# Kernel optimization log

Hardware: AMD Instinct MI355X
Metric: run time of the kernel (lower is better)

The kernel has to match this reference:

```python
import jax, jax.numpy as jnp
import numpy as np

N = 16384      # nodes per NodeFlow layer
E = 262144     # edges per block (avg degree 16)
T = 327680     # total interpro indices (~20 per node)
P = 20000      # protein embedding table rows
INTERPRO = 30000
D_ESM = 1280
D = 1024
L = 5000       # labels_num
G = 2          # num_gcn


def setup_inputs() -> dict:
    key = jax.random.key(0)
    ks = jax.random.split(key, 16)
    protein_embedding = jax.random.normal(ks[0], (P, D_ESM), jnp.float32) * 0.02
    interpro_weight = jax.random.normal(ks[1], (INTERPRO, D), jnp.float32) * 0.02
    W_esm = jax.random.normal(ks[2], (D, D_ESM), jnp.float32) * (1.0 / np.sqrt(D_ESM))
    b_esm = jnp.zeros((D,), jnp.float32)
    bias1 = jnp.zeros((D,), jnp.float32)
    bias2 = jnp.zeros((D,), jnp.float32)
    w = jnp.ones((2,), jnp.float32)
    W_upd = jax.random.normal(ks[3], (G, D, 2 * D), jnp.float32) * (1.0 / np.sqrt(2 * D))
    b_upd = jnp.zeros((G, D), jnp.float32)
    W_out = jax.random.normal(ks[4], (L, D + D_ESM), jnp.float32) * (1.0 / np.sqrt(D + D_ESM))
    b_out = jnp.zeros((L,), jnp.float32)
    self_w = jax.random.uniform(ks[5], (E,), jnp.float32)
    ppi_w = jax.random.uniform(ks[6], (E,), jnp.float32)
    inputs = jax.random.randint(ks[7], (N,), 0, P)
    interpro_idx = jax.random.randint(ks[8], (T,), 0, INTERPRO)
    off = jnp.sort(jax.random.randint(ks[9], (N + 1,), 0, T))
    interpro_off = off.at[0].set(0).at[-1].set(T)  # include_last_offset convention
    src = jax.random.randint(ks[10], (E,), 0, N)
    dst = jax.random.randint(ks[11], (E,), 0, N)
    target_id = jax.random.randint(ks[12], (N,), 0, P)
    return dict(protein_embedding=protein_embedding, interpro_weight=interpro_weight,
                W_esm=W_esm, b_esm=b_esm, bias1=bias1, bias2=bias2, w=w,
                W_upd=W_upd, b_upd=b_upd, W_out=W_out, b_out=b_out,
                self_w=self_w, ppi_w=ppi_w, inputs=inputs,
                interpro_idx=interpro_idx, interpro_off=interpro_off,
                src=src, dst=dst, target_id=target_id)


def reference(protein_embedding, interpro_weight, W_esm, b_esm, bias1, bias2, w,
              W_upd, b_upd, W_out, b_out, self_w, ppi_w,
              inputs, interpro_idx, interpro_off, src, dst, target_id):
    # x1: ESM branch -> relu(Linear(esm[inputs]) + bias1)
    x1 = jax.nn.relu(protein_embedding[inputs] @ W_esm.T + b_esm + bias1)  # [N, D]
    # x2: EmbeddingBag(mode='sum', include_last_offset=True) + bias2
    seg = jnp.searchsorted(interpro_off, jnp.arange(T), side='right') - 1  # bag id per index
    bags = jax.ops.segment_sum(interpro_weight[interpro_idx], seg, num_segments=N)
    x2 = jax.nn.relu(bags + bias2)  # [N, D]
    # learned softmax mixture of the two branches
    sm = jax.nn.softmax(w)
    h = sm[0] * x1 + sm[1] * x2  # [N, D]
    # message passing layers: u_mul_e + sum for 'self' and 'ppi' edge weights,
    # then NodeUpdate: relu(Linear(cat(ppi_out, res))). Dropout is identity (eval).
    for i in range(G):
        msg = h[src]  # [E, D] irregular gather
        res = jax.ops.segment_sum(msg * self_w[:, None], dst, num_segments=N)
        ppi_out = jax.ops.segment_sum(msg * ppi_w[:, None], dst, num_segments=N)
        h = jax.nn.relu(jnp.concatenate([ppi_out, res], axis=1) @ W_upd[i].T + b_upd[i])
    last = jnp.concatenate([h, protein_embedding[target_id]], axis=1)  # [N, D+D_ESM]
    return last @ W_out.T + b_out  # [N, L]
```

## Files before the change

### kernel.cpp

```cpp
#include <hip/hip_runtime.h>

typedef unsigned short u16;
typedef u16 u16x4 __attribute__((ext_vector_type(4)));
typedef u16 u16x8 __attribute__((ext_vector_type(8)));
typedef float f32x4 __attribute__((ext_vector_type(4)));
typedef __bf16 bf16x8 __attribute__((ext_vector_type(8)));

#define NN 16384
#define EE 262144
#define DD 1024
#define DESM 1280
#define LL 5000
#define IPN 30000

static __device__ __forceinline__ u16 f2bf(float f) {
  unsigned u = __float_as_uint(f);
  u += 0x7FFF + ((u >> 16) & 1);
  return (u16)(u >> 16);
}
static __device__ __forceinline__ float bf2f(u16 h) {
  return __uint_as_float(((unsigned)h) << 16);
}

__global__ void cast_rows_k(const float* __restrict__ src, int scols,
                            const int* __restrict__ rowidx,
                            u16* __restrict__ dst, int dld, int dcol0,
                            int rows, int cols8 ) {
  long total = (long)rows * cols8;
  for (long i = blockIdx.x * (long)blockDim.x + threadIdx.x; i < total;
       i += (long)gridDim.x * blockDim.x) {
    int r = (int)(i / cols8);
    int k8 = (int)(i % cols8);
    int sr = rowidx ? rowidx[r] : r;
    const f32x4* s = (const f32x4*)(src + (size_t)sr * scols + (size_t)k8 * 8);
    f32x4 a = s[0], b = s[1];
    u16x8 o;
    o[0] = f2bf(a[0]); o[1] = f2bf(a[1]); o[2] = f2bf(a[2]); o[3] = f2bf(a[3]);
    o[4] = f2bf(b[0]); o[5] = f2bf(b[1]); o[6] = f2bf(b[2]); o[7] = f2bf(b[3]);
    *(u16x8*)(dst + (size_t)r * dld + dcol0 + (size_t)k8 * 8) = o;
  }
}

__global__ void embed_bag_k(const u16* __restrict__ W, const int* __restrict__ idx,
                            const int* __restrict__ off, const float* __restrict__ bias2,
                            u16* __restrict__ x2b) {
  int node = blockIdx.x * 2 + (threadIdx.x >> 7);
  int t = threadIdx.x & 127;
  int beg = off[node], end = off[node + 1];
  float a[8];
#pragma unroll
  for (int j = 0; j < 8; ++j) a[j] = 0.f;
  int p = beg;
  for (; p + 8 <= end; p += 8) {
    u16x8 v[8];
#pragma unroll
    for (int q = 0; q < 8; ++q)
      v[q] = *(const u16x8*)(W + (size_t)idx[p + q] * DD + t * 8);
#pragma unroll
    for (int q = 0; q < 8; ++q)
#pragma unroll
      for (int j = 0; j < 8; ++j) a[j] += bf2f(v[q][j]);
  }
  for (; p + 2 <= end; p += 2) {
    u16x8 v0 = *(const u16x8*)(W + (size_t)idx[p] * DD + t * 8);
    u16x8 v1 = *(const u16x8*)(W + (size_t)idx[p + 1] * DD + t * 8);
#pragma unroll
    for (int j = 0; j < 8; ++j) a[j] += bf2f(v0[j]) + bf2f(v1[j]);
  }
  if (p < end) {
    u16x8 v0 = *(const u16x8*)(W + (size_t)idx[p] * DD + t * 8);
#pragma unroll
    for (int j = 0; j < 8; ++j) a[j] += bf2f(v0[j]);
  }
  f32x4 b0 = *(const f32x4*)(bias2 + t * 8);
  f32x4 b1 = *(const f32x4*)(bias2 + t * 8 + 4);
  u16x8 o;
#pragma unroll
  for (int j = 0; j < 4; ++j) o[j] = f2bf(fmaxf(a[j] + b0[j], 0.f));
#pragma unroll
  for (int j = 0; j < 4; ++j) o[j + 4] = f2bf(fmaxf(a[j + 4] + b1[j], 0.f));
  *(u16x8*)(x2b + (size_t)node * DD + t * 8) = o;
}

__global__ void hist_k(const int* __restrict__ dst, int* __restrict__ counts) {
  int e = blockIdx.x * blockDim.x + threadIdx.x;
  if (e < EE) atomicAdd(&counts[dst[e]], 1);
}

__global__ void scan_k(const int* __restrict__ counts, int* __restrict__ row_off) {
  __shared__ int sh[256];
  int t = threadIdx.x;
  int s = 0;
  for (int i = 0; i < 64; ++i) s += counts[t * 64 + i];
  sh[t] = s;
  __syncthreads();
  if (t == 0) {
    int run = 0;
    for (int i = 0; i < 256; ++i) { int v = sh[i]; sh[i] = run; run += v; }
    row_off[NN] = run;
  }
  __syncthreads();
  int run = sh[t];
  for (int i = 0; i < 64; ++i) { row_off[t * 64 + i] = run; run += counts[t * 64 + i]; }
}

__global__ void scatter_k(const int* __restrict__ dst, const int* __restrict__ src,
                          const float* __restrict__ selfw, const float* __restrict__ ppiw,
                          int* __restrict__ cursor, int4* __restrict__ rec) {
  int e = blockIdx.x * blockDim.x + threadIdx.x;
  if (e < EE) {
    int pos = atomicAdd(&cursor[dst[e]], 1);
    int4 r;
    r.x = src[e];
    r.y = __float_as_int(selfw[e]);
    r.z = __float_as_int(ppiw[e]);
    r.w = 0;
    rec[pos] = r;
  }
}

__global__ void aggregate_k(const u16* __restrict__ h, const int* __restrict__ row_off,
                            const int4* __restrict__ rec, u16* __restrict__ cat) {
  int node = blockIdx.x * 2 + (threadIdx.x >> 7);
  int t = threadIdx.x & 127;
  int beg = row_off[node], end = row_off[node + 1];
  float res[8], ppi[8];
#pragma unroll
  for (int j = 0; j < 8; ++j) { res[j] = 0.f; ppi[j] = 0.f; }
  int p = beg;
  for (; p + 8 <= end; p += 8) {
    int4 r[8];
    u16x8 m[8];
#pragma unroll
    for (int q = 0; q < 8; ++q) r[q] = rec[p + q];
#pragma unroll
    for (int q = 0; q < 8; ++q)
      m[q] = *(const u16x8*)(h + (size_t)r[q].x * DD + t * 8);
#pragma unroll
    for (int q = 0; q < 8; ++q) {
      float ws = __int_as_float(r[q].y), wp = __int_as_float(r[q].z);
#pragma unroll
      for (int j = 0; j < 8; ++j) {
        float f = bf2f(m[q][j]);
        res[j] += ws * f;
        ppi[j] += wp * f;
      }
    }
  }
  for (; p + 2 <= end; p += 2) {
    int4 r0 = rec[p], r1 = rec[p + 1];
    u16x8 m0 = *(const u16x8*)(h + (size_t)r0.x * DD + t * 8);
    u16x8 m1 = *(const u16x8*)(h + (size_t)r1.x * DD + t * 8);
    float ws0 = __int_as_float(r0.y), wp0 = __int_as_float(r0.z);
    float ws1 = __int_as_float(r1.y), wp1 = __int_as_float(r1.z);
#pragma unroll
    for (int j = 0; j < 8; ++j) {
      float f0 = bf2f(m0[j]), f1 = bf2f(m1[j]);
      res[j] += ws0 * f0 + ws1 * f1;
      ppi[j] += wp0 * f0 + wp1 * f1;
    }
  }
  if (p < end) {
    int4 r0 = rec[p];
    u16x8 m0 = *(const u16x8*)(h + (size_t)r0.x * DD + t * 8);
    float ws = __int_as_float(r0.y), wp = __int_as_float(r0.z);
#pragma unroll
    for (int j = 0; j < 8; ++j) {
      float f = bf2f(m0[j]);
      res[j] += ws * f;
      ppi[j] += wp * f;
    }
  }
  u16x8 o0, o1;
#pragma unroll
  for (int j = 0; j < 8; ++j) { o0[j] = f2bf(ppi[j]); o1[j] = f2bf(res[j]); }
  *(u16x8*)(cat + (size_t)node * 2048 + t * 8) = o0;
  *(u16x8*)(cat + (size_t)node * 2048 + DD + t * 8) = o1;
}

static __device__ __forceinline__ void stage_half(const char* Gb, size_t ldb, int rowbase,
                                                  int rowmax, int kbyte, char* lds_half_w,
                                                  int s_rowoff, int s_inner) {
#pragma unroll
  for (int j = 0; j < 2; ++j) {
    int row = rowbase + j * 128 + s_rowoff;
    if (row > rowmax) row = rowmax;
    const char* src = Gb + (size_t)row * ldb + kbyte + s_inner;
    __builtin_amdgcn_global_load_lds(
        (const __attribute__((address_space(1))) void*)src,
        (__attribute__((address_space(3))) void*)(lds_half_w + j * 8192), 16, 0, 0);
  }
}

static __device__ __forceinline__ bf16x8 ldr(const char* kh, int row, int slot) {
  unsigned a = (unsigned)row * 64u +
               ((((unsigned)slot << 4) ^ ((((unsigned)row >> 1) & 3u) << 4)));
  return *(const bf16x8*)(kh + a);
}

template <int MODE>
__global__ __launch_bounds__(512, 2) void gemm8_k(
    const u16* __restrict__ A, const u16* __restrict__ B, int M, int N, int K,
    void* __restrict__ Cout, int ldc, const float* __restrict__ bias0,
    const float* __restrict__ bias1, const u16* __restrict__ x2b,
    const float* __restrict__ wmix) {
  __shared__ char lds[131072];
  char* ldsA = lds;
  char* ldsB = lds + 65536;
  const int tid = threadIdx.x;
  const int lane = tid & 63;
  const int wid = tid >> 6;
  const int wr = wid >> 2;
  const int wc = wid & 3;
  const int nwg = gridDim.x * gridDim.y;
  const int flat = blockIdx.x + gridDim.x * blockIdx.y;
  const int swz = (flat & 7) * (nwg >> 3) + (flat >> 3);
  const int row0 = (swz / gridDim.x) * 256;
  const int col0 = (swz % gridDim.x) * 256;
  const int NT = K >> 6;
  const size_t lda = (size_t)K * 2;
  const char* Ab = (const char*)A;
  const char* Bb = (const char*)B;
  const int l15 = lane & 15;
  const int slot = lane >> 4;
  const int s_rowoff = wid * 16 + (lane >> 2);
  const int s_inner = (((lane & 3) << 4) ^ (((lane >> 3) & 3) << 4));
  const int wb = wid * 1024;

  f32x4 acc[8][4];
#pragma unroll
  for (int m = 0; m < 8; ++m)
#pragma unroll
    for (int n = 0; n < 4; ++n) acc[m][n] = (f32x4){0.f, 0.f, 0.f, 0.f};

  const int k1 = (NT > 1) ? 128 : 0;
  stage_half(Bb, lda, col0, N - 1, 0,       ldsB + 0     + wb, s_rowoff, s_inner);
  stage_half(Ab, lda, row0, M - 1, 0,       ldsA + 0     + wb, s_rowoff, s_inner);
  stage_half(Ab, lda, row0, M - 1, 64,      ldsA + 16384 + wb, s_rowoff, s_inner);
  stage_half(Bb, lda, col0, N - 1, 64,      ldsB + 16384 + wb, s_rowoff, s_inner);
  stage_half(Bb, lda, col0, N - 1, k1,      ldsB + 32768 + wb, s_rowoff, s_inner);
  stage_half(Ab, lda, row0, M - 1, k1,      ldsA + 32768 + wb, s_rowoff, s_inner);
  stage_half(Bb, lda, col0, N - 1, k1 + 64, ldsB + 49152 + wb, s_rowoff, s_inner);
  asm volatile("s_waitcnt vmcnt(6)" ::: "memory");
  __builtin_amdgcn_s_barrier();

  bf16x8 afP[4], afQ[4], bqP[4], bqQ[4];
#pragma unroll
  for (int m = 0; m < 4; ++m) afP[m] = ldr(ldsA, wr * 128 + m * 16 + l15, slot);
#pragma unroll
  for (int n = 0; n < 4; ++n) bqP[n] = ldr(ldsB, wc * 64 + n * 16 + l15, slot);

  for (int t = 0; t < NT; ++t) {
    const int d = t & 1;
    char* Ad = ldsA + d * 32768;
    char* Bd = ldsB + d * 32768;
    const char* Akh1 = Ad + 16384;
    const char* Bkh1 = Bd + 16384;
    const char* AkhN0 = ldsA + (d ^ 1) * 32768;
    const char* BkhN0 = ldsB + (d ^ 1) * 32768;
    const int ts1 = (t + 1 < NT) ? t + 1 : NT - 1;
    const int ts2 = (t + 2 < NT) ? t + 2 : NT - 1;

#pragma unroll
    for (int m = 0; m < 4; ++m) afQ[m] = ldr(Ad, wr * 128 + (m + 4) * 16 + l15, slot);
#pragma unroll
    for (int n = 0; n < 4; ++n) bqQ[n] = ldr(Bkh1, wc * 64 + n * 16 + l15, slot);
    stage_half(Ab, lda, row0, M - 1, ts1 * 128 + 64,
               ldsA + ((t + 1) & 1) * 32768 + 16384 + wb, s_rowoff, s_inner);
    __builtin_amdgcn_sched_barrier(0);
    __builtin_amdgcn_s_setprio(1);
#pragma unroll
    for (int m = 0; m < 4; ++m)
#pragma unroll
      for (int n = 0; n < 4; ++n)
        acc[m][n] = __builtin_amdgcn_mfma_f32_16x16x32_bf16(afP[m], bqP[n], acc[m][n], 0, 0, 0);
    __builtin_amdgcn_s_setprio(0);
    asm volatile("s_waitcnt vmcnt(8)" ::: "memory");
    __builtin_amdgcn_s_barrier();

#pragma unroll
    for (int m = 0; m < 4; ++m) afP[m] = ldr(Akh1, wr * 128 + (m + 4) * 16 + l15, slot);
    stage_half(Bb, lda, col0, N - 1, ts2 * 128, Bd + wb, s_rowoff, s_inner);
    __builtin_amdgcn_sched_barrier(0);
    __builtin_amdgcn_s_setprio(1);
#pragma unroll
    for (int m = 0; m < 4; ++m)
#pragma unroll
      for (int n = 0; n < 4; ++n)
        acc[m + 4][n] = __builtin_amdgcn_mfma_f32_16x16x32_bf16(afQ[m], bqP[n], acc[m + 4][n], 0, 0, 0);
    __builtin_amdgcn_s_setprio(0);
    __builtin_amdgcn_s_barrier();

#pragma unroll
    for (int m = 0; m < 4; ++m) afQ[m] = ldr(Akh1, wr * 128 + m * 16 + l15, slot);
    stage_half(Ab, lda, row0, M - 1, ts2 * 128, Ad + wb, s_rowoff, s_inner);
    __builtin_amdgcn_sched_barrier(0);
    __builtin_amdgcn_s_setprio(1);
#pragma unroll
    for (int m = 0; m < 4; ++m)
#pragma unroll
      for (int n = 0; n < 4; ++n)
        acc[m + 4][n] = __builtin_amdgcn_mfma_f32_16x16x32_bf16(afP[m], bqQ[n], acc[m + 4][n], 0, 0, 0);
    __builtin_amdgcn_s_setprio(0);
    asm volatile("s_waitcnt vmcnt(6)" ::: "memory");
    __builtin_amdgcn_s_barrier();

#pragma unroll
    for (int m = 0; m < 4; ++m) afP[m] = ldr(AkhN0, wr * 128 + m * 16 + l15, slot);
#pragma unroll
    for (int n = 0; n < 4; ++n) bqP[n] = ldr(BkhN0, wc * 64 + n * 16 + l15, slot);
    stage_half(Bb, lda, col0, N - 1, ts2 * 128 + 64, Bd + 16384 + wb, s_rowoff, s_inner);
    __builtin_amdgcn_sched_barrier(0);
    __builtin_amdgcn_s_setprio(1);
#pragma unroll
    for (int m = 0; m < 4; ++m)
#pragma unroll
      for (int n = 0; n < 4; ++n)
        acc[m][n] = __builtin_amdgcn_mfma_f32_16x16x32_bf16(afQ[m], bqQ[n], acc[m][n], 0, 0, 0);
    __builtin_amdgcn_s_setprio(0);
    __builtin_amdgcn_s_barrier();
  }

  float sm0 = 0.f, sm1 = 0.f;
  if (MODE == 0) {
    float w0 = wmix[0], w1 = wmix[1];
    float mx = fmaxf(w0, w1);
    float e0 = expf(w0 - mx), e1 = expf(w1 - mx);
    float inv = 1.f / (e0 + e1);
    sm0 = e0 * inv;
    sm1 = e1 * inv;
  }
  float bc[4];
  int cs[4];
#pragma unroll
  for (int n = 0; n < 4; ++n) {
    int c = col0 + wc * 64 + n * 16 + l15;
    cs[n] = c;
    bc[n] = (MODE == 2 && c >= N) ? 0.f : (bias0[c] + (MODE == 0 ? bias1[c] : 0.f));
  }
#pragma unroll
  for (int m = 0; m < 8; ++m) {
#pragma unroll
    for (int n = 0; n < 4; ++n) {
      int c = cs[n];
      if (MODE == 2 && c >= N) continue;
      int r0 = row0 + wr * 128 + m * 16 + slot * 4;
#pragma unroll
      for (int r = 0; r < 4; ++r) {
        float v = acc[m][n][r] + bc[n];
        int rr = r0 + r;
        if (MODE == 0) {
          float x1v = fmaxf(v, 0.f);
          float x2v = bf2f(x2b[(size_t)rr * DD + c]);
          ((u16*)Cout)[(size_t)rr * ldc + c] = f2bf(sm0 * x1v + sm1 * x2v);
        } else if (MODE == 1) {
          ((u16*)Cout)[(size_t)rr * ldc + c] = f2bf(fmaxf(v, 0.f));
        } else {
          __builtin_nontemporal_store(v, &((float*)Cout)[(size_t)rr * ldc + c]);
        }
      }
    }
  }
}

extern "C" void kernel_launch(void* const* d_in, const int* in_sizes, int n_in,
                              void* d_out, int out_size, void* d_ws, size_t ws_size,
                              hipStream_t stream) {
  const float* esm   = (const float*)d_in[0];
  const float* ipw   = (const float*)d_in[1];
  const float* Wesm  = (const float*)d_in[2];
  const float* besm  = (const float*)d_in[3];
  const float* bias1 = (const float*)d_in[4];
  const float* bias2 = (const float*)d_in[5];
  const float* wmix  = (const float*)d_in[6];
  const float* Wupd  = (const float*)d_in[7];
  const float* bupd  = (const float*)d_in[8];
  const float* Wout  = (const float*)d_in[9];
  const float* bout  = (const float*)d_in[10];
  const float* selfw = (const float*)d_in[11];
  const float* ppiw  = (const float*)d_in[12];
  const int* inputs  = (const int*)d_in[13];
  const int* ipidx   = (const int*)d_in[14];
  const int* ipoff   = (const int*)d_in[15];
  const int* src     = (const int*)d_in[16];
  const int* dst     = (const int*)d_in[17];
  const int* tgt     = (const int*)d_in[18];
  float* out = (float*)d_out;

  char* ws = (char*)d_ws;
  size_t o = 0;
  auto take = [&](size_t b) {
    char* r = ws + o;
    o += (b + 255) & ~(size_t)255;
    return r;
  };
  u16* Wesm_b = (u16*)take(1024ull * 1280 * 2);
  u16* Wupd_b = (u16*)take(2ull * 1024 * 2048 * 2);
  u16* Wout_b = (u16*)take(5000ull * 2304 * 2);
  int* counts  = (int*)take((size_t)NN * 4);
  int* row_off = (int*)take((size_t)(NN + 1) * 4);
  int* cursor  = (int*)take((size_t)NN * 4);
  int4* rec    = (int4*)take((size_t)EE * 16);
  u16* h_b     = (u16*)take((size_t)NN * DD * 2);
  char* shared0 = ws + o;
  size_t x2_b = ((size_t)NN * DD * 2 + 255) & ~(size_t)255;
  size_t a1_b = ((size_t)NN * DESM * 2 + 255) & ~(size_t)255;
  u16* x2b    = (u16*)shared0;
  u16* A1     = (u16*)(shared0 + x2_b);
  u16* ipw_b  = (u16*)(shared0 + x2_b + a1_b);
  u16* cat_b  = (u16*)shared0;
  u16* A_last = (u16*)(shared0 + x2_b + a1_b);

  cast_rows_k<<<2048, 256, 0, stream>>>(Wesm, 1280, nullptr, Wesm_b, 1280, 0, 1024, 160);
  cast_rows_k<<<2048, 256, 0, stream>>>(Wupd, 2048, nullptr, Wupd_b, 2048, 0, 2048, 256);
  cast_rows_k<<<2048, 256, 0, stream>>>(Wout, 2304, nullptr, Wout_b, 2304, 0, 5000, 288);
  cast_rows_k<<<4096, 256, 0, stream>>>(ipw, 1024, nullptr, ipw_b, 1024, 0, IPN, 128);

  embed_bag_k<<<NN / 2, 256, 0, stream>>>(ipw_b, ipidx, ipoff, bias2, x2b);

  cast_rows_k<<<4096, 256, 0, stream>>>(esm, 1280, inputs, A1, 1280, 0, NN, 160);

  hipMemsetAsync(counts, 0, (size_t)NN * 4, stream);
  hist_k<<<EE / 256, 256, 0, stream>>>(dst, counts);
  scan_k<<<1, 256, 0, stream>>>(counts, row_off);
  hipMemcpyAsync(cursor, row_off, (size_t)NN * 4, hipMemcpyDeviceToDevice, stream);
  scatter_k<<<EE / 256, 256, 0, stream>>>(dst, src, selfw, ppiw, cursor, rec);

  gemm8_k<0><<<dim3(4, 64), 512, 0, stream>>>(A1, Wesm_b, NN, 1024, 1280, h_b, 1024,
                                              besm, bias1, x2b, wmix);

  cast_rows_k<<<4096, 256, 0, stream>>>(esm, 1280, tgt, A_last, 2304, 1024, NN, 160);

  aggregate_k<<<NN / 2, 256, 0, stream>>>(h_b, row_off, rec, cat_b);
  gemm8_k<1><<<dim3(4, 64), 512, 0, stream>>>(cat_b, Wupd_b, NN, 1024, 2048, h_b, 1024,
                                              bupd, nullptr, nullptr, nullptr);

  aggregate_k<<<NN / 2, 256, 0, stream>>>(h_b, row_off, rec, cat_b);
  gemm8_k<1><<<dim3(4, 64), 512, 0, stream>>>(cat_b, Wupd_b + (size_t)1024 * 2048, NN, 1024,
                                              2048, A_last, 2304, bupd + 1024, nullptr,
                                              nullptr, nullptr);

  gemm8_k<2><<<dim3(20, 64), 512, 0, stream>>>(A_last, Wout_b, NN, 5000, 2304, out, 5000,
                                               bout, nullptr, nullptr, nullptr);
}
```

Before: 989.0 us.

## Restage GEMM LDS tiles by row halves with 128-byte rows and XOR swizzle

Changes the GEMM shared-memory layout. Each K-tile is now stored as two row halves with full 128-byte rows and an 8-way XOR swizzle, where before it was split into two 64-byte K halves. The staging order, the fragment-read addressing and the vmcnt waits are reworked to match. The aim is fewer LDS bank conflicts and wider contiguous global loads, at the cost of a different dependency ordering that could expose load latency. The fp32 output store also changes from nontemporal to a regular store.

```diff
diff --git a/kernel.cpp b/kernel.cpp
--- a/kernel.cpp
+++ b/kernel.cpp
@@ -179,23 +179,22 @@
 }
 
 static __device__ __forceinline__ void stage_half(const char* Gb, size_t ldb, int rowbase,
-                                                  int rowmax, int kbyte, char* lds_half_w,
+                                                  int rowmax, int kbyte, char* lds_dest_wb,
                                                   int s_rowoff, int s_inner) {
 #pragma unroll
   for (int j = 0; j < 2; ++j) {
-    int row = rowbase + j * 128 + s_rowoff;
+    int row = rowbase + j * 64 + s_rowoff;
     if (row > rowmax) row = rowmax;
     const char* src = Gb + (size_t)row * ldb + kbyte + s_inner;
     __builtin_amdgcn_global_load_lds(
         (const __attribute__((address_space(1))) void*)src,
-        (__attribute__((address_space(3))) void*)(lds_half_w + j * 8192), 16, 0, 0);
-  }
-}
-
-static __device__ __forceinline__ bf16x8 ldr(const char* kh, int row, int slot) {
-  unsigned a = (unsigned)row * 64u +
-               ((((unsigned)slot << 4) ^ ((((unsigned)row >> 1) & 3u) << 4)));
-  return *(const bf16x8*)(kh + a);
+        (__attribute__((address_space(3))) void*)(lds_dest_wb + j * 8192), 16, 0, 0);
+  }
+}
+
+static __device__ __forceinline__ bf16x8 ldr2(const char* base, int row, int kk, int slot) {
+  unsigned g = ((unsigned)(kk * 4 + slot)) ^ ((unsigned)row & 7u);
+  return *(const bf16x8*)(base + (unsigned)row * 128u + g * 16u);
 }
 
 template <int MODE>
@@ -223,8 +222,8 @@
   const char* Bb = (const char*)B;
   const int l15 = lane & 15;
   const int slot = lane >> 4;
-  const int s_rowoff = wid * 16 + (lane >> 2);
-  const int s_inner = (((lane & 3) << 4) ^ (((lane >> 3) & 3) << 4));
+  const int s_rowoff = wid * 8 + (lane >> 3);
+  const int s_inner = (((lane & 7) ^ ((lane >> 3) & 7)) << 4);
   const int wb = wid * 1024;
 
   f32x4 acc[8][4];
@@ -234,38 +233,36 @@
     for (int n = 0; n < 4; ++n) acc[m][n] = (f32x4){0.f, 0.f, 0.f, 0.f};
 
   const int k1 = (NT > 1) ? 128 : 0;
-  stage_half(Bb, lda, col0, N - 1, 0,       ldsB + 0     + wb, s_rowoff, s_inner);
-  stage_half(Ab, lda, row0, M - 1, 0,       ldsA + 0     + wb, s_rowoff, s_inner);
-  stage_half(Ab, lda, row0, M - 1, 64,      ldsA + 16384 + wb, s_rowoff, s_inner);
-  stage_half(Bb, lda, col0, N - 1, 64,      ldsB + 16384 + wb, s_rowoff, s_inner);
-  stage_half(Bb, lda, col0, N - 1, k1,      ldsB + 32768 + wb, s_rowoff, s_inner);
-  stage_half(Ab, lda, row0, M - 1, k1,      ldsA + 32768 + wb, s_rowoff, s_inner);
-  stage_half(Bb, lda, col0, N - 1, k1 + 64, ldsB + 49152 + wb, s_rowoff, s_inner);
+  stage_half(Bb, lda, col0,       N - 1, 0,  ldsB + 0     + wb, s_rowoff, s_inner);
+  stage_half(Bb, lda, col0 + 128, N - 1, 0,  ldsB + 16384 + wb, s_rowoff, s_inner);
+  stage_half(Ab, lda, row0,       M - 1, 0,  ldsA + 0     + wb, s_rowoff, s_inner);
+  stage_half(Ab, lda, row0 + 128, M - 1, 0,  ldsA + 16384 + wb, s_rowoff, s_inner);
+  stage_half(Bb, lda, col0,       N - 1, k1, ldsB + 32768 + wb, s_rowoff, s_inner);
+  stage_half(Bb, lda, col0 + 128, N - 1, k1, ldsB + 49152 + wb, s_rowoff, s_inner);
+  stage_half(Ab, lda, row0,       M - 1, k1, ldsA + 32768 + wb, s_rowoff, s_inner);
   asm volatile("s_waitcnt vmcnt(6)" ::: "memory");
   __builtin_amdgcn_s_barrier();
 
   bf16x8 afP[4], afQ[4], bqP[4], bqQ[4];
 #pragma unroll
-  for (int m = 0; m < 4; ++m) afP[m] = ldr(ldsA, wr * 128 + m * 16 + l15, slot);
-#pragma unroll
-  for (int n = 0; n < 4; ++n) bqP[n] = ldr(ldsB, wc * 64 + n * 16 + l15, slot);
+  for (int m = 0; m < 4; ++m) afP[m] = ldr2(ldsA, wr * 128 + m * 16 + l15, 0, slot);
+#pragma unroll
+  for (int n = 0; n < 4; ++n) bqP[n] = ldr2(ldsB, wc * 64 + n * 16 + l15, 0, slot);
 
   for (int t = 0; t < NT; ++t) {
     const int d = t & 1;
     char* Ad = ldsA + d * 32768;
     char* Bd = ldsB + d * 32768;
-    const char* Akh1 = Ad + 16384;
-    const char* Bkh1 = Bd + 16384;
-    const char* AkhN0 = ldsA + (d ^ 1) * 32768;
-    const char* BkhN0 = ldsB + (d ^ 1) * 32768;
+    char* AdN = ldsA + (d ^ 1) * 32768;
+    char* BdN = ldsB + (d ^ 1) * 32768;
     const int ts1 = (t + 1 < NT) ? t + 1 : NT - 1;
     const int ts2 = (t + 2 < NT) ? t + 2 : NT - 1;
 
 #pragma unroll
-    for (int m = 0; m < 4; ++m) afQ[m] = ldr(Ad, wr * 128 + (m + 4) * 16 + l15, slot);
-#pragma unroll
-    for (int n = 0; n < 4; ++n) bqQ[n] = ldr(Bkh1, wc * 64 + n * 16 + l15, slot);
-    stage_half(Ab, lda, row0, M - 1, ts1 * 128 + 64,
+    for (int m = 0; m < 4; ++m) afQ[m] = ldr2(Ad, wr * 128 + (m + 4) * 16 + l15, 0, slot);
+#pragma unroll
+    for (int n = 0; n < 4; ++n) bqQ[n] = ldr2(Bd, wc * 64 + n * 16 + l15, 1, slot);
+    stage_half(Ab, lda, row0 + 128, M - 1, ts1 * 128,
                ldsA + ((t + 1) & 1) * 32768 + 16384 + wb, s_rowoff, s_inner);
     __builtin_amdgcn_sched_barrier(0);
     __builtin_amdgcn_s_setprio(1);
@@ -275,11 +272,10 @@
       for (int n = 0; n < 4; ++n)
         acc[m][n] = __builtin_amdgcn_mfma_f32_16x16x32_bf16(afP[m], bqP[n], acc[m][n], 0, 0, 0);
     __builtin_amdgcn_s_setprio(0);
-    asm volatile("s_waitcnt vmcnt(8)" ::: "memory");
     __builtin_amdgcn_s_barrier();
 
 #pragma unroll
-    for (int m = 0; m < 4; ++m) afP[m] = ldr(Akh1, wr * 128 + (m + 4) * 16 + l15, slot);
+    for (int m = 0; m < 4; ++m) afP[m] = ldr2(Ad, wr * 128 + (m + 4) * 16 + l15, 1, slot);
     stage_half(Bb, lda, col0, N - 1, ts2 * 128, Bd + wb, s_rowoff, s_inner);
     __builtin_amdgcn_sched_barrier(0);
     __builtin_amdgcn_s_setprio(1);
@@ -292,8 +288,8 @@
     __builtin_amdgcn_s_barrier();
 
 #pragma unroll
-    for (int m = 0; m < 4; ++m) afQ[m] = ldr(Akh1, wr * 128 + m * 16 + l15, slot);
-    stage_half(Ab, lda, row0, M - 1, ts2 * 128, Ad + wb, s_rowoff, s_inner);
+    for (int m = 0; m < 4; ++m) afQ[m] = ldr2(Ad, wr * 128 + m * 16 + l15, 1, slot);
+    stage_half(Bb, lda, col0 + 128, N - 1, ts2 * 128, Bd + 16384 + wb, s_rowoff, s_inner);
     __builtin_amdgcn_sched_barrier(0);
     __builtin_amdgcn_s_setprio(1);
 #pragma unroll
@@ -302,14 +298,14 @@
       for (int n = 0; n < 4; ++n)
         acc[m + 4][n] = __builtin_amdgcn_mfma_f32_16x16x32_bf16(afP[m], bqQ[n], acc[m + 4][n], 0, 0, 0);
     __builtin_amdgcn_s_setprio(0);
-    asm volatile("s_waitcnt vmcnt(6)" ::: "memory");
+    asm volatile("s_waitcnt vmcnt(4)" ::: "memory");
     __builtin_amdgcn_s_barrier();
 
 #pragma unroll
-    for (int m = 0; m < 4; ++m) afP[m] = ldr(AkhN0, wr * 128 + m * 16 + l15, slot);
-#pragma unroll
-    for (int n = 0; n < 4; ++n) bqP[n] = ldr(BkhN0, wc * 64 + n * 16 + l15, slot);
-    stage_half(Bb, lda, col0, N - 1, ts2 * 128 + 64, Bd + 16384 + wb, s_rowoff, s_inner);
+    for (int m = 0; m < 4; ++m) afP[m] = ldr2(AdN, wr * 128 + m * 16 + l15, 0, slot);
+#pragma unroll
+    for (int n = 0; n < 4; ++n) bqP[n] = ldr2(BdN, wc * 64 + n * 16 + l15, 0, slot);
+    stage_half(Ab, lda, row0, M - 1, ts2 * 128, Ad + wb, s_rowoff, s_inner);
     __builtin_amdgcn_sched_barrier(0);
     __builtin_amdgcn_s_setprio(1);
 #pragma unroll
@@ -356,7 +352,7 @@
         } else if (MODE == 1) {
           ((u16*)Cout)[(size_t)rr * ldc + c] = f2bf(fmaxf(v, 0.f));
         } else {
-          __builtin_nontemporal_store(v, &((float*)Cout)[(size_t)rr * ldc + c]);
+          ((float*)Cout)[(size_t)rr * ldc + c] = v;
         }
       }
     }
```

After: 900.2 us. 9.0% less time.
